# Kernel optimization log

Measured on AMD Instinct MI355X. Metric: run time of the kernel, lower is better.

Reference implementation:

```python
import jax, jax.numpy as jnp
import numpy as np

EPS = 1e-9
# i = 7,6,...,-1 use exp_factor = -(4**i); i = -2 uses 0.0 (matches torch's reversed(range(-2,8)))
EXP_FACTORS = np.array([-(4.0 ** i) for i in range(7, -2, -1)] + [0.0], dtype=np.float32)


def setup_inputs() -> dict:
    key = jax.random.key(0)
    k1, k2 = jax.random.split(key)
    B, N, D = 16, 2048, 3
    preds = jax.random.normal(k1, (B, N, D), dtype=jnp.float32)
    labels = jax.random.normal(k2, (B, N, D), dtype=jnp.float32)
    return {"preds": preds, "labels": labels}


def _pairwise_dist(p1, p2):
    # ||p1||^2 + ||p2||^2 - 2 p1 . p2  -> [B, N, N]
    p1n = jnp.sum(p1 * p1, axis=-1)[..., :, None]
    p2n = jnp.sum(p2 * p2, axis=-1)[..., None, :]
    return p1n + p2n - 2.0 * jnp.einsum('bnd,bmd->bnm', p1, p2)


def _approx_match(pwdist):
    B, N, _ = pwdist.shape
    match0 = jnp.zeros_like(pwdist)
    cost0 = jnp.ones((B, 1, N), dtype=pwdist.dtype)      # per-target remaining capacity
    curr0 = jnp.ones((B, N, 1), dtype=pwdist.dtype)      # per-source remaining currency

    def step(carry, ef):
        match, cost, currency = carry
        bids = jnp.exp(ef * pwdist) * cost
        bids = bids * currency / (jnp.sum(bids, axis=1, keepdims=True) + EPS)
        bid_wt = jnp.minimum(cost / (jnp.sum(bids, axis=1, keepdims=True) + EPS), 1.0)
        bids = bids * bid_wt
        match = match + bids
        cost = jnp.maximum(cost - jnp.sum(bids, axis=1, keepdims=True), 0.0)
        currency = jnp.maximum(currency - jnp.sum(bids, axis=2, keepdims=True), 0.0)
        return (match, cost, currency), None

    (match, _, _), _ = jax.lax.scan(step, (match0, cost0, curr0), jnp.asarray(EXP_FACTORS))
    return match


def reference(preds, labels):
    pwdist = _pairwise_dist(preds, labels)
    match = _approx_match(pwdist)
    return jnp.sum(match * pwdist)
```

## Files before the change

### kernel.cpp

```cpp
#include <hip/hip_runtime.h>
#include <cstddef>

#define BB    16
#define NN    2048
#define BN    (BB * NN)
#define EPSF  1e-9f
#define TPB   512
#define CPT   2
#define SPLIT 16
#define TILE  128
#define CHUNK 1024

extern "C" __device__ float __ocml_native_exp2_f32(float);
__device__ __forceinline__ float fast_exp2(float x) {
#if __has_builtin(__builtin_amdgcn_exp2f)
    return __builtin_amdgcn_exp2f(x);
#else
    return __ocml_native_exp2_f32(x);
#endif
}

__global__ __launch_bounds__(TPB, 4) void passA(
    const float* __restrict__ preds, const float* __restrict__ labels,
    const float* __restrict__ curprev, float* __restrict__ curout,
    const float* __restrict__ RSprev, const float* __restrict__ RRprev,
    float* __restrict__ RSz, float* __restrict__ RRz,
    float* __restrict__ Sacc, float* __restrict__ Tacc,
    float* __restrict__ out, float c1, int k)
{
    __shared__ float4 s_p[TILE];
    __shared__ float  s_cu[TILE];
    __shared__ float  s_red[2];
    int blk = blockIdx.x;
    int split = blk & 15, mc = (blk >> 4) & 1, b = blk >> 5;
    int t = threadIdx.x;
    int base = b * NN;

    if (t < TILE) {
        int idx = base + split * TILE + t;
        const float* p = preds + (size_t)idx * 3;
        float px = p[0], py = p[1], pz = p[2];
        float pn = px * px + py * py + pz * pz;
        float cu, contrib = 0.0f;
        if (k == 0) cu = 1.0f;
        else {
            float cup = curprev[idx], rs = RSprev[idx], rr = RRprev[idx];
            contrib = cup * rr;
            cu = fmaxf(cup * (1.0f - rs), 0.0f);
        }
        s_p[t]  = make_float4(px, py, pz, c1 * pn);
        s_cu[t] = cu;
        if (mc == 0) {
            curout[idx] = cu;
            RSz[idx] = 0.0f; RRz[idx] = 0.0f;
        }
        if (k > 0 && mc == 0) {
#pragma unroll
            for (int o = 32; o > 0; o >>= 1) contrib += __shfl_down(contrib, o, 64);
            if ((t & 63) == 0) s_red[t >> 6] = contrib;
        }
    }

    int m0 = mc * CHUNK + t;
    float gx[CPT], gy[CPT], gz[CPT], am[CPT], Sa[CPT], Ta[CPT];
    float n2c1 = -2.0f * c1;
#pragma unroll
    for (int c = 0; c < CPT; c++) {
        int m = m0 + c * TPB;
        const float* l = labels + (size_t)(base + m) * 3;
        float lx = l[0], ly = l[1], lz = l[2];
        gx[c] = n2c1 * lx; gy[c] = n2c1 * ly; gz[c] = n2c1 * lz;
        am[c] = c1 * (lx * lx + ly * ly + lz * lz);
        Sa[c] = 0.0f; Ta[c] = 0.0f;
    }
    __syncthreads();
    if (k > 0 && mc == 0 && t == 0) atomicAdd(out, s_red[0] + s_red[1]);

#pragma unroll 8
    for (int j = 0; j < TILE; j++) {
        float4 P = s_p[j]; float cu = s_cu[j];
#pragma unroll
        for (int c = 0; c < CPT; c++) {
            float arg = fmaf(P.x, gx[c], fmaf(P.y, gy[c], fmaf(P.z, gz[c], P.w + am[c])));
            float e = fast_exp2(arg);
            Sa[c] += e;
            Ta[c] = fmaf(e, cu, Ta[c]);
        }
    }
#pragma unroll
    for (int c = 0; c < CPT; c++) {
        int idx = base + m0 + c * TPB;
        atomicAdd(&Sacc[idx], Sa[c]);
        atomicAdd(&Tacc[idx], Ta[c]);
    }
}

__global__ __launch_bounds__(TPB, 4) void passB(
    const float* __restrict__ preds, const float* __restrict__ labels,
    const float* __restrict__ Sread, const float* __restrict__ Tread,
    const float* __restrict__ costprev, float* __restrict__ costout,
    float* __restrict__ Sz, float* __restrict__ Tz,
    float* __restrict__ RSacc, float* __restrict__ RRacc,
    float c1, float invc1, int k, int last)
{
    __shared__ float4 s_l[TILE];
    __shared__ float  s_cc[TILE];
    int blk = blockIdx.x;
    int split = blk & 15, nc = (blk >> 4) & 1, b = blk >> 5;
    int t = threadIdx.x;
    int base = b * NN;

    if (t < TILE) {
        int idx = base + split * TILE + t;
        const float* l = labels + (size_t)idx * 3;
        float lx = l[0], ly = l[1], lz = l[2];
        float lm2 = lx * lx + ly * ly + lz * lz;
        float S = Sread[idx], T = Tread[idx];
        float cost = (k == 0) ? 1.0f : costprev[idx];
        float D1 = fmaf(cost, S, EPSF);
        float S2 = cost * T / D1;
        float bw = fminf(cost / (S2 + EPSF), 1.0f);
        float cc = cost * bw / D1;
        if (nc == 0) {
            costout[idx] = fmaxf(fmaf(-S2, bw, cost), 0.0f);
            Sz[idx] = 0.0f; Tz[idx] = 0.0f;
        }
        if (last) s_l[t] = make_float4(lx, ly, lz, lm2);
        else      s_l[t] = make_float4(-2.0f * c1 * lx, -2.0f * c1 * ly,
                                       -2.0f * c1 * lz, c1 * lm2);
        s_cc[t] = cc;
    }

    int n0 = nc * CHUNK + t;
    float px[CPT], py[CPT], pz[CPT], qq[CPT], RSa[CPT], RRa[CPT];
#pragma unroll
    for (int c = 0; c < CPT; c++) {
        int n = n0 + c * TPB;
        const float* p = preds + (size_t)(base + n) * 3;
        px[c] = p[0]; py[c] = p[1]; pz[c] = p[2];
        float pn = px[c] * px[c] + py[c] * py[c] + pz[c] * pz[c];
        qq[c] = last ? pn : c1 * pn;
        RSa[c] = 0.0f; RRa[c] = 0.0f;
    }
    __syncthreads();

    if (!last) {
#pragma unroll 8
        for (int j = 0; j < TILE; j++) {
            float4 L = s_l[j]; float ccj = s_cc[j];
#pragma unroll
            for (int c = 0; c < CPT; c++) {
                float arg = fmaf(px[c], L.x, fmaf(py[c], L.y, fmaf(pz[c], L.z, qq[c] + L.w)));
                float e = fast_exp2(arg);
                float w = e * ccj;
                RSa[c] += w;
                RRa[c] = fmaf(w, arg, RRa[c]);
            }
        }
#pragma unroll
        for (int c = 0; c < CPT; c++) {
            int idx = base + n0 + c * TPB;
            atomicAdd(&RSacc[idx], RSa[c]);
            atomicAdd(&RRacc[idx], RRa[c] * invc1);
        }
    } else {
#pragma unroll 8
        for (int j = 0; j < TILE; j++) {
            float4 L = s_l[j]; float ccj = s_cc[j];
#pragma unroll
            for (int c = 0; c < CPT; c++) {
                float dot = fmaf(px[c], L.x, fmaf(py[c], L.y, pz[c] * L.z));
                float pw  = fmaf(-2.0f, dot, qq[c] + L.w);
                RRa[c] = fmaf(ccj, pw, RRa[c]);
            }
        }
#pragma unroll
        for (int c = 0; c < CPT; c++) {
            int idx = base + n0 + c * TPB;
            atomicAdd(&RRacc[idx], RRa[c]);
        }
    }
}

__global__ void finalK(const float* __restrict__ cur, const float* __restrict__ RR,
                       float* __restrict__ out)
{
    int t = threadIdx.x;
    int i = blockIdx.x * TPB + t;
    float contrib = cur[i] * RR[i];
#pragma unroll
    for (int o = 32; o > 0; o >>= 1) contrib += __shfl_down(contrib, o, 64);
    __shared__ float s_red[TPB / 64];
    if ((t & 63) == 0) s_red[t >> 6] = contrib;
    __syncthreads();
    if (t == 0) {
        float s = 0.0f;
#pragma unroll
        for (int w = 0; w < TPB / 64; w++) s += s_red[w];
        atomicAdd(out, s);
    }
}

extern "C" void kernel_launch(void* const* d_in, const int* in_sizes, int n_in,
                              void* d_out, int out_size, void* d_ws, size_t ws_size,
                              hipStream_t stream) {
    const float* preds  = (const float*)d_in[0];
    const float* labels = (const float*)d_in[1];
    float* out = (float*)d_out;
    float* ws  = (float*)d_ws;

    float* S[2]     = {ws + 0 * BN, ws + 2 * BN};
    float* T[2]     = {ws + 1 * BN, ws + 3 * BN};
    float* RS[2]    = {ws + 4 * BN, ws + 6 * BN};
    float* RR[2]    = {ws + 5 * BN, ws + 7 * BN};
    float* curb[2]  = {ws + 8 * BN, ws + 9 * BN};
    float* costb[2] = {ws + 10 * BN, ws + 11 * BN};

    hipMemsetAsync(d_out, 0, sizeof(float), stream);
    hipMemsetAsync(ws, 0, (size_t)2 * BN * sizeof(float), stream);

    static const float efs[10] = {-16384.0f, -4096.0f, -1024.0f, -256.0f, -64.0f,
                                  -16.0f, -4.0f, -1.0f, -0.25f, 0.0f};
    const float log2e = 1.44269504088896f;
    for (int k = 0; k < 10; k++) {
        float c1 = efs[k] * log2e;
        float invc1 = (efs[k] != 0.0f) ? 1.0f / c1 : 0.0f;
        int pk = k & 1, pp = (k + 1) & 1;
        passA<<<512, TPB, 0, stream>>>(preds, labels,
            curb[pp], curb[pk],
            RS[pp], RR[pp],
            RS[pk], RR[pk],
            S[pk], T[pk],
            out, c1, k);
        passB<<<512, TPB, 0, stream>>>(preds, labels,
            S[pk], T[pk],
            costb[pk], costb[pp],
            S[pp], T[pp],
            RS[pk], RR[pk],
            c1, invc1, k, (k == 9) ? 1 : 0);
    }
    finalK<<<BN / TPB, TPB, 0, stream>>>(curb[1], RR[1], out);
}
```

Before: 351.6 us.

## Replace atomic accumulation with per-split partial buffers and packed float2 math

Each block now writes its column sums into a per-split partial array instead of issuing atomicAdds, and the next pass reduces the 32 partials in shared memory. This removes the atomics, the zeroing writes and the initial memset. Blocks drop to 256 threads with 8 columns per thread handled as float2 pairs, aiming at packed FMA, over 64-row tiles. The cost is more global traffic from reading SPLIT partials per element and a much larger workspace.

After: 405.4 us. +15.3%, slower.

```diff
diff --git a/kernel.cpp b/kernel.cpp
--- a/kernel.cpp
+++ b/kernel.cpp
@@ -5,198 +5,250 @@
 #define NN    2048
 #define BN    (BB * NN)
 #define EPSF  1e-9f
-#define TPB   512
-#define CPT   2
-#define SPLIT 16
-#define TILE  128
-#define CHUNK 1024
-
-extern "C" __device__ float __ocml_native_exp2_f32(float);
+#define TPB   256
+#define NPAIR 4
+#define SPLIT 32
+#define TILE  64
+#define PIDX(s, b, i) ((((size_t)(s)) * BB + (b)) * NN + (i))
+
+typedef float f2 __attribute__((ext_vector_type(2)));
+
 __device__ __forceinline__ float fast_exp2(float x) {
 #if __has_builtin(__builtin_amdgcn_exp2f)
     return __builtin_amdgcn_exp2f(x);
 #else
-    return __ocml_native_exp2_f32(x);
+    return exp2f(x);
 #endif
 }
 
-__global__ __launch_bounds__(TPB, 4) void passA(
+__global__ __launch_bounds__(TPB) void passA(
     const float* __restrict__ preds, const float* __restrict__ labels,
     const float* __restrict__ curprev, float* __restrict__ curout,
-    const float* __restrict__ RSprev, const float* __restrict__ RRprev,
-    float* __restrict__ RSz, float* __restrict__ RRz,
-    float* __restrict__ Sacc, float* __restrict__ Tacc,
+    const float* __restrict__ RSp, const float* __restrict__ RRp,
+    float* __restrict__ Sp, float* __restrict__ Tp,
     float* __restrict__ out, float c1, int k)
 {
     __shared__ float4 s_p[TILE];
     __shared__ float  s_cu[TILE];
-    __shared__ float  s_red[2];
+    __shared__ float  s_ws[2][4][TILE];
     int blk = blockIdx.x;
-    int split = blk & 15, mc = (blk >> 4) & 1, b = blk >> 5;
+    int split = blk & (SPLIT - 1), b = blk >> 5;
     int t = threadIdx.x;
     int base = b * NN;
+    int r = t & (TILE - 1), w = t >> 6;
+
+    if (k > 0) {
+        float aRS = 0.f, aRR = 0.f;
+#pragma unroll
+        for (int s8 = 0; s8 < SPLIT / 4; s8++) {
+            int s = w * (SPLIT / 4) + s8;
+            aRS += RSp[PIDX(s, b, split * TILE + r)];
+            aRR += RRp[PIDX(s, b, split * TILE + r)];
+        }
+        s_ws[0][w][r] = aRS;
+        s_ws[1][w][r] = aRR;
+    }
+    __syncthreads();
 
     if (t < TILE) {
         int idx = base + split * TILE + t;
         const float* p = preds + (size_t)idx * 3;
         float px = p[0], py = p[1], pz = p[2];
         float pn = px * px + py * py + pz * pz;
-        float cu, contrib = 0.0f;
-        if (k == 0) cu = 1.0f;
+        float cu, contrib = 0.f;
+        if (k == 0) cu = 1.f;
         else {
-            float cup = curprev[idx], rs = RSprev[idx], rr = RRprev[idx];
+            float rs = s_ws[0][0][t] + s_ws[0][1][t] + s_ws[0][2][t] + s_ws[0][3][t];
+            float rr = s_ws[1][0][t] + s_ws[1][1][t] + s_ws[1][2][t] + s_ws[1][3][t];
+            float cup = curprev[idx];
             contrib = cup * rr;
-            cu = fmaxf(cup * (1.0f - rs), 0.0f);
+            cu = fmaxf(cup * (1.f - rs), 0.f);
         }
         s_p[t]  = make_float4(px, py, pz, c1 * pn);
         s_cu[t] = cu;
-        if (mc == 0) {
-            curout[idx] = cu;
-            RSz[idx] = 0.0f; RRz[idx] = 0.0f;
-        }
-        if (k > 0 && mc == 0) {
+        curout[idx] = cu;
+        if (k > 0) {
 #pragma unroll
             for (int o = 32; o > 0; o >>= 1) contrib += __shfl_down(contrib, o, 64);
-            if ((t & 63) == 0) s_red[t >> 6] = contrib;
-        }
-    }
-
-    int m0 = mc * CHUNK + t;
-    float gx[CPT], gy[CPT], gz[CPT], am[CPT], Sa[CPT], Ta[CPT];
-    float n2c1 = -2.0f * c1;
-#pragma unroll
-    for (int c = 0; c < CPT; c++) {
-        int m = m0 + c * TPB;
-        const float* l = labels + (size_t)(base + m) * 3;
-        float lx = l[0], ly = l[1], lz = l[2];
-        gx[c] = n2c1 * lx; gy[c] = n2c1 * ly; gz[c] = n2c1 * lz;
-        am[c] = c1 * (lx * lx + ly * ly + lz * lz);
-        Sa[c] = 0.0f; Ta[c] = 0.0f;
-    }
-    __syncthreads();
-    if (k > 0 && mc == 0 && t == 0) atomicAdd(out, s_red[0] + s_red[1]);
-
-#pragma unroll 8
+            if (t == 0) atomicAdd(out, contrib);
+        }
+    }
+
+    f2 gx[NPAIR], gy[NPAIR], gz[NPAIR], am[NPAIR], Sa[NPAIR], Ta[NPAIR];
+    float n2c1 = -2.f * c1;
+#pragma unroll
+    for (int p = 0; p < NPAIR; p++) {
+        int m0 = t + (2 * p) * TPB, m1 = t + (2 * p + 1) * TPB;
+        const float* l0 = labels + (size_t)(base + m0) * 3;
+        const float* l1 = labels + (size_t)(base + m1) * 3;
+        float ax = l0[0], ay = l0[1], az = l0[2];
+        float bx = l1[0], by = l1[1], bz = l1[2];
+        gx[p] = (f2){n2c1 * ax, n2c1 * bx};
+        gy[p] = (f2){n2c1 * ay, n2c1 * by};
+        gz[p] = (f2){n2c1 * az, n2c1 * bz};
+        am[p] = (f2){c1 * (ax * ax + ay * ay + az * az),
+                     c1 * (bx * bx + by * by + bz * bz)};
+        Sa[p] = (f2){0.f, 0.f};
+        Ta[p] = (f2){0.f, 0.f};
+    }
+    __syncthreads();
+
+#pragma unroll 4
     for (int j = 0; j < TILE; j++) {
-        float4 P = s_p[j]; float cu = s_cu[j];
-#pragma unroll
-        for (int c = 0; c < CPT; c++) {
-            float arg = fmaf(P.x, gx[c], fmaf(P.y, gy[c], fmaf(P.z, gz[c], P.w + am[c])));
-            float e = fast_exp2(arg);
-            Sa[c] += e;
-            Ta[c] = fmaf(e, cu, Ta[c]);
-        }
-    }
-#pragma unroll
-    for (int c = 0; c < CPT; c++) {
-        int idx = base + m0 + c * TPB;
-        atomicAdd(&Sacc[idx], Sa[c]);
-        atomicAdd(&Tacc[idx], Ta[c]);
-    }
-}
-
-__global__ __launch_bounds__(TPB, 4) void passB(
+        float4 P = s_p[j];
+        float cuj = s_cu[j];
+#pragma unroll
+        for (int p = 0; p < NPAIR; p++) {
+            f2 arg = P.x * gx[p] + (P.y * gy[p] + (P.z * gz[p] + (am[p] + P.w)));
+            f2 e;
+            e.x = fast_exp2(arg.x);
+            e.y = fast_exp2(arg.y);
+            Sa[p] += e;
+            Ta[p] += e * cuj;
+        }
+    }
+#pragma unroll
+    for (int p = 0; p < NPAIR; p++) {
+        int m0 = t + (2 * p) * TPB, m1 = t + (2 * p + 1) * TPB;
+        Sp[PIDX(split, b, m0)] = Sa[p].x;
+        Sp[PIDX(split, b, m1)] = Sa[p].y;
+        Tp[PIDX(split, b, m0)] = Ta[p].x;
+        Tp[PIDX(split, b, m1)] = Ta[p].y;
+    }
+}
+
+__global__ __launch_bounds__(TPB) void passB(
     const float* __restrict__ preds, const float* __restrict__ labels,
-    const float* __restrict__ Sread, const float* __restrict__ Tread,
+    const float* __restrict__ Sp, const float* __restrict__ Tp,
     const float* __restrict__ costprev, float* __restrict__ costout,
-    float* __restrict__ Sz, float* __restrict__ Tz,
-    float* __restrict__ RSacc, float* __restrict__ RRacc,
+    float* __restrict__ RSp, float* __restrict__ RRp,
     float c1, float invc1, int k, int last)
 {
     __shared__ float4 s_l[TILE];
     __shared__ float  s_cc[TILE];
+    __shared__ float  s_ws[2][4][TILE];
     int blk = blockIdx.x;
-    int split = blk & 15, nc = (blk >> 4) & 1, b = blk >> 5;
+    int split = blk & (SPLIT - 1), b = blk >> 5;
     int t = threadIdx.x;
     int base = b * NN;
+    int r = t & (TILE - 1), w = t >> 6;
+
+    {
+        float aS = 0.f, aT = 0.f;
+#pragma unroll
+        for (int s8 = 0; s8 < SPLIT / 4; s8++) {
+            int s = w * (SPLIT / 4) + s8;
+            aS += Sp[PIDX(s, b, split * TILE + r)];
+            aT += Tp[PIDX(s, b, split * TILE + r)];
+        }
+        s_ws[0][w][r] = aS;
+        s_ws[1][w][r] = aT;
+    }
+    __syncthreads();
 
     if (t < TILE) {
         int idx = base + split * TILE + t;
-        const float* l = labels + (size_t)idx * 3;
+        const float* l = preds ? labels + (size_t)idx * 3 : nullptr;
         float lx = l[0], ly = l[1], lz = l[2];
         float lm2 = lx * lx + ly * ly + lz * lz;
-        float S = Sread[idx], T = Tread[idx];
-        float cost = (k == 0) ? 1.0f : costprev[idx];
+        float S = s_ws[0][0][t] + s_ws[0][1][t] + s_ws[0][2][t] + s_ws[0][3][t];
+        float T = s_ws[1][0][t] + s_ws[1][1][t] + s_ws[1][2][t] + s_ws[1][3][t];
+        float cost = (k == 0) ? 1.f : costprev[idx];
         float D1 = fmaf(cost, S, EPSF);
         float S2 = cost * T / D1;
-        float bw = fminf(cost / (S2 + EPSF), 1.0f);
+        float bw = fminf(cost / (S2 + EPSF), 1.f);
         float cc = cost * bw / D1;
-        if (nc == 0) {
-            costout[idx] = fmaxf(fmaf(-S2, bw, cost), 0.0f);
-            Sz[idx] = 0.0f; Tz[idx] = 0.0f;
-        }
+        costout[idx] = fmaxf(fmaf(-S2, bw, cost), 0.f);
         if (last) s_l[t] = make_float4(lx, ly, lz, lm2);
-        else      s_l[t] = make_float4(-2.0f * c1 * lx, -2.0f * c1 * ly,
-                                       -2.0f * c1 * lz, c1 * lm2);
+        else      s_l[t] = make_float4(-2.f * c1 * lx, -2.f * c1 * ly,
+                                       -2.f * c1 * lz, c1 * lm2);
         s_cc[t] = cc;
     }
 
-    int n0 = nc * CHUNK + t;
-    float px[CPT], py[CPT], pz[CPT], qq[CPT], RSa[CPT], RRa[CPT];
-#pragma unroll
-    for (int c = 0; c < CPT; c++) {
-        int n = n0 + c * TPB;
-        const float* p = preds + (size_t)(base + n) * 3;
-        px[c] = p[0]; py[c] = p[1]; pz[c] = p[2];
-        float pn = px[c] * px[c] + py[c] * py[c] + pz[c] * pz[c];
-        qq[c] = last ? pn : c1 * pn;
-        RSa[c] = 0.0f; RRa[c] = 0.0f;
+    f2 qx[NPAIR], qy[NPAIR], qz[NPAIR], qn[NPAIR], RSa[NPAIR], RRa[NPAIR];
+#pragma unroll
+    for (int p = 0; p < NPAIR; p++) {
+        int n0 = t + (2 * p) * TPB, n1 = t + (2 * p + 1) * TPB;
+        const float* p0 = preds + (size_t)(base + n0) * 3;
+        const float* p1 = preds + (size_t)(base + n1) * 3;
+        float ax = p0[0], ay = p0[1], az = p0[2];
+        float bx = p1[0], by = p1[1], bz = p1[2];
+        qx[p] = (f2){ax, bx};
+        qy[p] = (f2){ay, by};
+        qz[p] = (f2){az, bz};
+        float pn0 = ax * ax + ay * ay + az * az;
+        float pn1 = bx * bx + by * by + bz * bz;
+        qn[p] = last ? (f2){pn0, pn1} : (f2){c1 * pn0, c1 * pn1};
+        RSa[p] = (f2){0.f, 0.f};
+        RRa[p] = (f2){0.f, 0.f};
     }
     __syncthreads();
 
     if (!last) {
-#pragma unroll 8
+#pragma unroll 4
         for (int j = 0; j < TILE; j++) {
-            float4 L = s_l[j]; float ccj = s_cc[j];
-#pragma unroll
-            for (int c = 0; c < CPT; c++) {
-                float arg = fmaf(px[c], L.x, fmaf(py[c], L.y, fmaf(pz[c], L.z, qq[c] + L.w)));
-                float e = fast_exp2(arg);
-                float w = e * ccj;
-                RSa[c] += w;
-                RRa[c] = fmaf(w, arg, RRa[c]);
+            float4 L = s_l[j];
+            float ccj = s_cc[j];
+#pragma unroll
+            for (int p = 0; p < NPAIR; p++) {
+                f2 arg = qx[p] * L.x + (qy[p] * L.y + (qz[p] * L.z + (qn[p] + L.w)));
+                f2 e;
+                e.x = fast_exp2(arg.x);
+                e.y = fast_exp2(arg.y);
+                f2 wv = e * ccj;
+                RSa[p] += wv;
+                RRa[p] += wv * arg;
             }
         }
 #pragma unroll
-        for (int c = 0; c < CPT; c++) {
-            int idx = base + n0 + c * TPB;
-            atomicAdd(&RSacc[idx], RSa[c]);
-            atomicAdd(&RRacc[idx], RRa[c] * invc1);
+        for (int p = 0; p < NPAIR; p++) {
+            int n0 = t + (2 * p) * TPB, n1 = t + (2 * p + 1) * TPB;
+            RSp[PIDX(split, b, n0)] = RSa[p].x;
+            RSp[PIDX(split, b, n1)] = RSa[p].y;
+            RRp[PIDX(split, b, n0)] = RRa[p].x * invc1;
+            RRp[PIDX(split, b, n1)] = RRa[p].y * invc1;
         }
     } else {
-#pragma unroll 8
+#pragma unroll 4
         for (int j = 0; j < TILE; j++) {
-            float4 L = s_l[j]; float ccj = s_cc[j];
-#pragma unroll
-            for (int c = 0; c < CPT; c++) {
-                float dot = fmaf(px[c], L.x, fmaf(py[c], L.y, pz[c] * L.z));
-                float pw  = fmaf(-2.0f, dot, qq[c] + L.w);
-                RRa[c] = fmaf(ccj, pw, RRa[c]);
+            float4 L = s_l[j];
+            float ccj = s_cc[j];
+#pragma unroll
+            for (int p = 0; p < NPAIR; p++) {
+                f2 dot = qx[p] * L.x + (qy[p] * L.y + qz[p] * L.z);
+                f2 pw  = (qn[p] + L.w) - 2.f * dot;
+                RRa[p] += ccj * pw;
             }
         }
 #pragma unroll
-        for (int c = 0; c < CPT; c++) {
-            int idx = base + n0 + c * TPB;
-            atomicAdd(&RRacc[idx], RRa[c]);
-        }
-    }
-}
-
-__global__ void finalK(const float* __restrict__ cur, const float* __restrict__ RR,
-                       float* __restrict__ out)
+        for (int p = 0; p < NPAIR; p++) {
+            int n0 = t + (2 * p) * TPB, n1 = t + (2 * p + 1) * TPB;
+            RRp[PIDX(split, b, n0)] = RRa[p].x;
+            RRp[PIDX(split, b, n1)] = RRa[p].y;
+        }
+    }
+}
+
+__global__ __launch_bounds__(TPB) void finalK(const float* __restrict__ cur,
+                                              const float* __restrict__ RRp,
+                                              float* __restrict__ out)
 {
     int t = threadIdx.x;
     int i = blockIdx.x * TPB + t;
-    float contrib = cur[i] * RR[i];
+    int b = i >> 11, n = i & (NN - 1);
+    float acc = 0.f;
+#pragma unroll
+    for (int s = 0; s < SPLIT; s++) acc += RRp[PIDX(s, b, n)];
+    float contrib = cur[i] * acc;
 #pragma unroll
     for (int o = 32; o > 0; o >>= 1) contrib += __shfl_down(contrib, o, 64);
     __shared__ float s_red[TPB / 64];
     if ((t & 63) == 0) s_red[t >> 6] = contrib;
     __syncthreads();
     if (t == 0) {
-        float s = 0.0f;
-#pragma unroll
-        for (int w = 0; w < TPB / 64; w++) s += s_red[w];
+        float s = 0.f;
+#pragma unroll
+        for (int wv = 0; wv < TPB / 64; wv++) s += s_red[wv];
         atomicAdd(out, s);
     }
 }
@@ -209,35 +261,31 @@
     float* out = (float*)d_out;
     float* ws  = (float*)d_ws;
 
-    float* S[2]     = {ws + 0 * BN, ws + 2 * BN};
-    float* T[2]     = {ws + 1 * BN, ws + 3 * BN};
-    float* RS[2]    = {ws + 4 * BN, ws + 6 * BN};
-    float* RR[2]    = {ws + 5 * BN, ws + 7 * BN};
-    float* curb[2]  = {ws + 8 * BN, ws + 9 * BN};
-    float* costb[2] = {ws + 10 * BN, ws + 11 * BN};
+    const size_t PSZ = (size_t)SPLIT * BB * NN;
+    float* Sp  = ws;
+    float* Tp  = ws + PSZ;
+    float* RSp = ws + 2 * PSZ;
+    float* RRp = ws + 3 * PSZ;
+    float* curb[2]  = {ws + 4 * PSZ,          ws + 4 * PSZ + BN};
+    float* costb[2] = {ws + 4 * PSZ + 2 * BN, ws + 4 * PSZ + 3 * BN};
 
     hipMemsetAsync(d_out, 0, sizeof(float), stream);
-    hipMemsetAsync(ws, 0, (size_t)2 * BN * sizeof(float), stream);
 
     static const float efs[10] = {-16384.0f, -4096.0f, -1024.0f, -256.0f, -64.0f,
                                   -16.0f, -4.0f, -1.0f, -0.25f, 0.0f};
     const float log2e = 1.44269504088896f;
+    const int grid = BB * SPLIT;
     for (int k = 0; k < 10; k++) {
         float c1 = efs[k] * log2e;
         float invc1 = (efs[k] != 0.0f) ? 1.0f / c1 : 0.0f;
-        int pk = k & 1, pp = (k + 1) & 1;
-        passA<<<512, TPB, 0, stream>>>(preds, labels,
-            curb[pp], curb[pk],
-            RS[pp], RR[pp],
-            RS[pk], RR[pk],
-            S[pk], T[pk],
-            out, c1, k);
-        passB<<<512, TPB, 0, stream>>>(preds, labels,
-            S[pk], T[pk],
-            costb[pk], costb[pp],
-            S[pp], T[pp],
-            RS[pk], RR[pk],
+        passA<<<grid, TPB, 0, stream>>>(preds, labels,
+            curb[(k + 1) & 1], curb[k & 1],
+            RSp, RRp, Sp, Tp, out, c1, k);
+        passB<<<grid, TPB, 0, stream>>>(preds, labels,
+            Sp, Tp,
+            costb[k & 1], costb[(k + 1) & 1],
+            RSp, RRp,
             c1, invc1, k, (k == 9) ? 1 : 0);
     }
-    finalK<<<BN / TPB, TPB, 0, stream>>>(curb[1], RR[1], out);
-}
+    finalK<<<BN / TPB, TPB, 0, stream>>>(curb[1], RRp, out);
+}
```
